# Optimization experiments

Hardware: AMD Instinct MI355X
Metric: run time of the kernel (lower is better)

## Reference

```python
import jax, jax.numpy as jnp
import numpy as np

HIDDEN_DIM = 1024
NUM_HEADS = 16
HEAD_DIM = HIDDEN_DIM // NUM_HEADS
SCALAR_NORM = float(np.sqrt(HIDDEN_DIM / NUM_HEADS))


def setup_inputs() -> dict:
    key = jax.random.key(0)
    k1, k2 = jax.random.split(key)
    B, N, D = 2, 2048, HIDDEN_DIM
    x = jax.random.normal(k1, (B, N, D), dtype=jnp.float32)
    # torch Linear weight shape: (3D, D); xavier_uniform-like scale
    limit = float(np.sqrt(6.0 / (D + 3 * D)))
    W_qkv = jax.random.uniform(k2, (3 * D, D), dtype=jnp.float32, minval=-limit, maxval=limit)
    return {"x": x, "W_qkv": W_qkv}


def reference(x, W_qkv):
    b, n, d = x.shape
    h, hd = NUM_HEADS, HEAD_DIM
    qkv = x @ W_qkv.T  # (B, N, 3D)
    q, k, v = jnp.split(qkv, 3, axis=-1)
    # (B, H, N, hd)
    q = q.reshape(b, n, h, hd).transpose(0, 2, 1, 3)
    k = k.reshape(b, n, h, hd).transpose(0, 2, 1, 3)
    v = v.reshape(b, n, h, hd).transpose(0, 2, 1, 3)
    scores = jnp.einsum('bhik,bhjk->bhij', q, k) / SCALAR_NORM
    attn = jax.nn.softmax(scores, axis=-1)
    out = jnp.einsum('bhij,bhjk->bhik', attn, v)
    return out.transpose(0, 2, 1, 3).reshape(b, n, d)
```

## Files before the change

kernel.cpp:

```cpp
#include <hip/hip_runtime.h>
#include <hip/hip_bf16.h>

#define SEQ 2048
#define DMODEL 1024
#define NHEADS 16
#define HD 64
#define BATCH 2

typedef short bf16x8 __attribute__((ext_vector_type(8)));
typedef float f32x4 __attribute__((ext_vector_type(4)));
typedef float f32x16 __attribute__((ext_vector_type(16)));

static __device__ inline ushort f2bf(float f) {
    unsigned u = __float_as_uint(f);
    return (ushort)((u + 0x7fffu + ((u >> 16) & 1u)) >> 16);
}

static __device__ inline unsigned pk2bf(float a, float b) {
    __hip_bfloat162 h = __float22bfloat162_rn(make_float2(a, b));
    union { __hip_bfloat162 h; unsigned u; } c; c.h = h;
    return c.u;
}

static __device__ inline void async16(const ushort* g, ushort* l) {
    __builtin_amdgcn_global_load_lds((const __attribute__((address_space(1))) void*)g,
                                     (__attribute__((address_space(3))) void*)l, 16, 0, 0);
}

static __device__ inline void plane32swap(unsigned& a, unsigned& b) {
    asm volatile("v_permlane32_swap_b32 %0, %1" : "+v"(a), "+v"(b));
}

__global__ void cvt2(const float* __restrict__ a, ushort* __restrict__ da, int na,
                     const float* __restrict__ b, ushort* __restrict__ db, int nb) {
    long i = (long)(blockIdx.x * blockDim.x + threadIdx.x) * 4;
    const float* s; ushort* d;
    if (i < na) { s = a + i; d = da + i; }
    else { long j = i - na; if (j >= nb) return; s = b + j; d = db + j; }
    float4 v = *(const float4*)s;
    ushort4 o; o.x = f2bf(v.x); o.y = f2bf(v.y); o.z = f2bf(v.z); o.w = f2bf(v.w);
    *(ushort4*)d = o;
}

union GemmSmem {
    struct { ushort A[128 * 64]; ushort B[128 * 64]; } st;
    ushort C[128 * 128];
};

__global__ __launch_bounds__(256) void qkv_gemm(
        const ushort* __restrict__ X, const ushort* __restrict__ W,
        ushort* __restrict__ Qd, ushort* __restrict__ Kd, ushort* __restrict__ Vd) {
    __shared__ GemmSmem sm;
    const int t = threadIdx.x;
    const int lane = t & 63, l15 = lane & 15, quad = lane >> 4;
    const int w = t >> 6, wm = w >> 1, wn = w & 1;
    const int gm = blockIdx.x, gn = blockIdx.y;
    const int srow = t >> 3, scol = (t & 7) * 8;

    f32x4 acc[4][4] = {};

    for (int kt = 0; kt < 16; ++kt) {
        const int k0 = kt * 64;
        __syncthreads();
#pragma unroll
        for (int inst = 0; inst < 4; ++inst) {
            async16(&X[(gm * 128 + inst * 32 + srow) * 1024 + k0 + scol], &sm.st.A[inst * 2048 + t * 8]);
            async16(&W[(gn * 128 + inst * 32 + srow) * 1024 + k0 + scol], &sm.st.B[inst * 2048 + t * 8]);
        }
        __syncthreads();
#pragma unroll
        for (int ks = 0; ks < 2; ++ks) {
            const int kk = ks * 32 + quad * 8;
            bf16x8 af[4], bfr[4];
#pragma unroll
            for (int i = 0; i < 4; ++i) {
                af[i]  = *(const bf16x8*)&sm.st.A[(wm * 64 + i * 16 + l15) * 64 + kk];
                bfr[i] = *(const bf16x8*)&sm.st.B[(wn * 64 + i * 16 + l15) * 64 + kk];
            }
#pragma unroll
            for (int i = 0; i < 4; ++i)
#pragma unroll
                for (int j = 0; j < 4; ++j)
                    acc[i][j] = __builtin_amdgcn_mfma_f32_16x16x32_bf16(af[i], bfr[j], acc[i][j], 0, 0, 0);
        }
    }

    __syncthreads();
    const float sc = (gn < 8) ? (0.125f * 1.44269504f) : 1.0f;
#pragma unroll
    for (int i = 0; i < 4; ++i)
#pragma unroll
        for (int reg = 0; reg < 4; ++reg) {
            const int row = wm * 64 + i * 16 + quad * 4 + reg;
            const int sw = (row & 7) * 8;
#pragma unroll
            for (int jp = 0; jp < 4; jp += 2) {
                unsigned u = pk2bf(acc[i][jp][reg] * sc, acc[i][jp + 1][reg] * sc);
                sm.C[row * 128 + ((wn * 64 + jp * 16 + l15) ^ sw)] = (ushort)u;
                sm.C[row * 128 + ((wn * 64 + (jp + 1) * 16 + l15) ^ sw)] = (ushort)(u >> 16);
            }
        }
    __syncthreads();

    const int which = gn >> 3;
    ushort* dst = (which == 0) ? Qd : ((which == 1) ? Kd : Vd);
    const int rloc = t >> 4, l = t & 15;
#pragma unroll
    for (int pass = 0; pass < 8; ++pass) {
        const int r = pass * 16 + rloc;
        bf16x8 v = *(const bf16x8*)&sm.C[r * 128 + ((l * 8) ^ ((r & 7) * 8))];
        const int ng = gm * 128 + r;
        const int b = ng >> 11, n = ng & 2047;
        const int cl = (gn * 128 + l * 8) & 1023;
        const int h = cl >> 6, hd = cl & 63;
        *(bf16x8*)&dst[(((b * NHEADS + h) * SEQ) + n) * HD + hd] = v;
    }
}

__global__ __launch_bounds__(256) void tr_v(const ushort* __restrict__ src, ushort* __restrict__ dst) {
    __shared__ ushort sT[64][72];
    const int t = threadIdx.x;
    const int bh = blockIdx.y, nt = blockIdx.x;
    const int r0 = t >> 3, c8 = (t & 7) * 8;
    const ushort* sp = src + ((long)bh * SEQ + nt * 64) * HD;
#pragma unroll
    for (int rr = 0; rr < 64; rr += 32)
        *(bf16x8*)&sT[rr + r0][c8] = *(const bf16x8*)&sp[(rr + r0) * HD + c8];
    __syncthreads();
    ushort* dp = dst + (long)bh * HD * SEQ + nt * 64;
#pragma unroll
    for (int rr = 0; rr < 64; rr += 32) {
        const int hd = rr + r0;
        bf16x8 v;
#pragma unroll
        for (int j = 0; j < 8; ++j) v[j] = (short)sT[c8 + j][hd];
        *(bf16x8*)&dp[(long)hd * SEQ + c8] = v;
    }
}

__global__ __launch_bounds__(256, 2) void attn_kernel(
        const ushort* __restrict__ Q, const ushort* __restrict__ K,
        const ushort* __restrict__ VT, float* __restrict__ O) {
    __shared__ ushort sK[2][128 * 64];
    __shared__ ushort sVT[2][64 * 128];
    __shared__ float sL[4][32];

    const int t = threadIdx.x;
    const int lane = t & 63, l31 = lane & 31, hi = lane >> 5;
    const int w = t >> 6;

    const int flat = blockIdx.y * gridDim.x + blockIdx.x;
    const int qt = (flat >> 3) & 15;
    const int bh = (flat & 7) + ((flat >> 7) << 3);

    const ushort* Qp = Q + ((long)bh * SEQ + qt * 128 + w * 32) * HD;
    const ushort* Kp = K + (long)bh * SEQ * HD;
    const ushort* Vp = VT + (long)bh * HD * SEQ;

    bf16x8 bq[4];
#pragma unroll
    for (int ks = 0; ks < 4; ++ks)
        bq[ks] = *(const bf16x8*)&Qp[l31 * HD + ks * 16 + hi * 8];

    const int krow = t >> 3;
    const int kcol = ((t & 7) ^ (krow & 7)) * 8;
    const ushort* gK = Kp + krow * HD + kcol;
    const int vrow = t >> 4;
    const int vcol = ((t & 15) ^ (vrow & 7)) * 8;
    const ushort* gV = Vp + (long)vrow * SEQ + vcol;

    ushort* lK[2] = { &sK[0][t * 8], &sK[1][t * 8] };
    ushort* lV[2] = { &sVT[0][t * 8], &sVT[1][t * 8] };

    f32x16 accO[2] = {};
    f32x4 Lp4 = {};
    const int swz = (l31 & 7) << 3;

#pragma unroll
    for (int c = 0; c < 4; ++c) {
        async16(gK + c * 32 * HD, lK[0] + c * 2048);
        async16(gV + (long)c * 16 * SEQ, lV[0] + c * 2048);
    }
    __syncthreads();

    for (int kt = 0; kt < 16; ++kt) {
        const int cur = kt & 1;
        if (kt < 15) {
            const ushort* nK = gK + (kt + 1) * 128 * HD;
            const ushort* nV = gV + (kt + 1) * 128;
#pragma unroll
            for (int c = 0; c < 4; ++c) {
                async16(nK + c * 32 * HD, lK[cur ^ 1] + c * 2048);
                async16(nV + (long)c * 16 * SEQ, lV[cur ^ 1] + c * 2048);
            }
        }
        const ushort* bK = sK[cur];
        const ushort* bV = sVT[cur];

        f32x16 s[4];
        __builtin_amdgcn_s_setprio(1);
#pragma unroll
        for (int nb = 0; nb < 4; ++nb) {
            f32x16 z = {};
#pragma unroll
            for (int ks = 0; ks < 4; ++ks) {
                bf16x8 ak = *(const bf16x8*)&bK[(nb * 32 + l31) * 64 + ((ks * 16 + hi * 8) ^ swz)];
                z = __builtin_amdgcn_mfma_f32_32x32x16_bf16(ak, bq[ks], z, 0, 0, 0);
            }
            s[nb] = z;
        }
        __builtin_amdgcn_s_setprio(0);

#pragma unroll
        for (int h = 0; h < 2; ++h) {
            bf16x8 pa[4];
#pragma unroll
            for (int nb = 0; nb < 2; ++nb) {
                float p[16];
#pragma unroll
                for (int r = 0; r < 16; ++r) p[r] = exp2f(s[h * 2 + nb][r]);
#pragma unroll
                for (int r = 0; r < 16; ++r) Lp4[r & 3] += p[r];
#pragma unroll
                for (int h2 = 0; h2 < 2; ++h2) {
                    const int b = 8 * h2;
                    unsigned c0 = pk2bf(p[b + 0], p[b + 1]);
                    unsigned c1 = pk2bf(p[b + 2], p[b + 3]);
                    unsigned c2 = pk2bf(p[b + 4], p[b + 5]);
                    unsigned c3 = pk2bf(p[b + 6], p[b + 7]);
                    plane32swap(c0, c2);
                    plane32swap(c1, c3);
                    union { unsigned u[4]; bf16x8 v; } f;
                    f.u[0] = c0; f.u[1] = c1; f.u[2] = c2; f.u[3] = c3;
                    pa[nb * 2 + h2] = f.v;
                }
            }
            __builtin_amdgcn_s_setprio(1);
#pragma unroll
            for (int db = 0; db < 2; ++db)
#pragma unroll
                for (int ks = 0; ks < 4; ++ks) {
                    bf16x8 vf = *(const bf16x8*)&bV[(db * 32 + l31) * 128 + h * 64 + ((ks * 16 + hi * 8) ^ swz)];
                    accO[db] = __builtin_amdgcn_mfma_f32_32x32x16_bf16(pa[ks], vf, accO[db], 0, 0, 0);
                }
            __builtin_amdgcn_s_setprio(0);
        }

        __syncthreads();
    }

    const float Lp = (Lp4[0] + Lp4[1]) + (Lp4[2] + Lp4[3]);
    unsigned lu = __float_as_uint(Lp), lv = lu;
    plane32swap(lu, lv);
    const float Ltot = __uint_as_float(lu) + __uint_as_float(lv);
    if (hi == 0) sL[w][l31] = Ltot;
    __syncthreads();

    const int b = bh >> 4, h = bh & 15;
    const int qg0 = qt * 128 + w * 32;
#pragma unroll
    for (int r = 0; r < 16; ++r) {
        const int ql = (r & 3) + 8 * (r >> 2) + 4 * hi;
        const float inv = 1.0f / sL[w][ql];
        const int row = qg0 + ql;
#pragma unroll
        for (int db = 0; db < 2; ++db)
            O[((long)b * SEQ + row) * DMODEL + h * HD + db * 32 + l31] = accO[db][r] * inv;
    }
}

extern "C" void kernel_launch(void* const* d_in, const int* in_sizes, int n_in,
                              void* d_out, int out_size, void* d_ws, size_t ws_size,
                              hipStream_t stream) {
    const float* x  = (const float*)d_in[0];
    const float* Wq = (const float*)d_in[1];
    float* out = (float*)d_out;

    const int NX = BATCH * SEQ * DMODEL;
    const int NW = 3 * DMODEL * DMODEL;
    const int NQKV = BATCH * NHEADS * SEQ * HD;

    ushort* xb = (ushort*)d_ws;
    ushort* wb = xb + NX;
    ushort* q  = wb + NW;
    ushort* k  = q + NQKV;
    ushort* vtmp = k + NQKV;
    ushort* vt = xb;

    cvt2<<<(NX + NW) / 4 / 256, 256, 0, stream>>>(x, xb, NX, Wq, wb, NW);

    dim3 g1(4096 / 128, 3072 / 128);
    qkv_gemm<<<g1, 256, 0, stream>>>(xb, wb, q, k, vtmp);

    dim3 gt(SEQ / 64, BATCH * NHEADS);
    tr_v<<<gt, 256, 0, stream>>>(vtmp, vt);

    dim3 g2(SEQ / 128, BATCH * NHEADS);
    attn_kernel<<<g2, 256, 0, stream>>>(q, k, vt, out);
}
```

Measured before the change: 177.7 us.

## Process two 32-row query blocks per wave to reuse K/V tile loads

```diff
diff --git a/kernel.cpp b/kernel.cpp
--- a/kernel.cpp
+++ b/kernel.cpp
@@ -138,29 +138,31 @@
     }
 }
 
-__global__ __launch_bounds__(256, 2) void attn_kernel(
+__global__ __launch_bounds__(256, 1) void attn_kernel(
         const ushort* __restrict__ Q, const ushort* __restrict__ K,
         const ushort* __restrict__ VT, float* __restrict__ O) {
     __shared__ ushort sK[2][128 * 64];
     __shared__ ushort sVT[2][64 * 128];
-    __shared__ float sL[4][32];
+    __shared__ float sL[4][64];
 
     const int t = threadIdx.x;
     const int lane = t & 63, l31 = lane & 31, hi = lane >> 5;
     const int w = t >> 6;
 
     const int flat = blockIdx.y * gridDim.x + blockIdx.x;
-    const int qt = (flat >> 3) & 15;
-    const int bh = (flat & 7) + ((flat >> 7) << 3);
-
-    const ushort* Qp = Q + ((long)bh * SEQ + qt * 128 + w * 32) * HD;
+    const int qt = (flat >> 3) & 7;
+    const int bh = (flat & 7) + ((flat >> 6) << 3);
+
+    const ushort* Qp = Q + ((long)bh * SEQ + qt * 256 + w * 64) * HD;
     const ushort* Kp = K + (long)bh * SEQ * HD;
     const ushort* Vp = VT + (long)bh * HD * SEQ;
 
-    bf16x8 bq[4];
-#pragma unroll
-    for (int ks = 0; ks < 4; ++ks)
-        bq[ks] = *(const bf16x8*)&Qp[l31 * HD + ks * 16 + hi * 8];
+    bf16x8 bq[2][4];
+#pragma unroll
+    for (int qh = 0; qh < 2; ++qh)
+#pragma unroll
+        for (int ks = 0; ks < 4; ++ks)
+            bq[qh][ks] = *(const bf16x8*)&Qp[(qh * 32 + l31) * HD + ks * 16 + hi * 8];
 
     const int krow = t >> 3;
     const int kcol = ((t & 7) ^ (krow & 7)) * 8;
@@ -172,8 +174,8 @@
     ushort* lK[2] = { &sK[0][t * 8], &sK[1][t * 8] };
     ushort* lV[2] = { &sVT[0][t * 8], &sVT[1][t * 8] };
 
-    f32x16 accO[2] = {};
-    f32x4 Lp4 = {};
+    f32x16 accA[2] = {}, accB[2] = {};
+    f32x4 LpA = {}, LpB = {};
     const int swz = (l31 & 7) << 3;
 
 #pragma unroll
@@ -197,75 +199,94 @@
         const ushort* bK = sK[cur];
         const ushort* bV = sVT[cur];
 
-        f32x16 s[4];
-        __builtin_amdgcn_s_setprio(1);
+        f32x16 sA[4], sB[4];
 #pragma unroll
         for (int nb = 0; nb < 4; ++nb) {
-            f32x16 z = {};
+            f32x16 zA = {}, zB = {};
 #pragma unroll
             for (int ks = 0; ks < 4; ++ks) {
                 bf16x8 ak = *(const bf16x8*)&bK[(nb * 32 + l31) * 64 + ((ks * 16 + hi * 8) ^ swz)];
-                z = __builtin_amdgcn_mfma_f32_32x32x16_bf16(ak, bq[ks], z, 0, 0, 0);
-            }
-            s[nb] = z;
-        }
-        __builtin_amdgcn_s_setprio(0);
+                zA = __builtin_amdgcn_mfma_f32_32x32x16_bf16(ak, bq[0][ks], zA, 0, 0, 0);
+                zB = __builtin_amdgcn_mfma_f32_32x32x16_bf16(ak, bq[1][ks], zB, 0, 0, 0);
+            }
+            sA[nb] = zA; sB[nb] = zB;
+        }
 
 #pragma unroll
         for (int h = 0; h < 2; ++h) {
-            bf16x8 pa[4];
-#pragma unroll
-            for (int nb = 0; nb < 2; ++nb) {
-                float p[16];
-#pragma unroll
-                for (int r = 0; r < 16; ++r) p[r] = exp2f(s[h * 2 + nb][r]);
-#pragma unroll
-                for (int r = 0; r < 16; ++r) Lp4[r & 3] += p[r];
+            bf16x8 paA[4], paB[4];
+#pragma unroll
+            for (int nb2 = 0; nb2 < 2; ++nb2) {
+                float pA[16], pB[16];
+#pragma unroll
+                for (int r = 0; r < 16; ++r) {
+                    pA[r] = __builtin_amdgcn_exp2f(sA[h * 2 + nb2][r]);
+                    pB[r] = __builtin_amdgcn_exp2f(sB[h * 2 + nb2][r]);
+                }
+#pragma unroll
+                for (int r = 0; r < 16; ++r) { LpA[r & 3] += pA[r]; LpB[r & 3] += pB[r]; }
 #pragma unroll
                 for (int h2 = 0; h2 < 2; ++h2) {
                     const int b = 8 * h2;
-                    unsigned c0 = pk2bf(p[b + 0], p[b + 1]);
-                    unsigned c1 = pk2bf(p[b + 2], p[b + 3]);
-                    unsigned c2 = pk2bf(p[b + 4], p[b + 5]);
-                    unsigned c3 = pk2bf(p[b + 6], p[b + 7]);
-                    plane32swap(c0, c2);
-                    plane32swap(c1, c3);
-                    union { unsigned u[4]; bf16x8 v; } f;
-                    f.u[0] = c0; f.u[1] = c1; f.u[2] = c2; f.u[3] = c3;
-                    pa[nb * 2 + h2] = f.v;
+                    unsigned a0 = pk2bf(pA[b + 0], pA[b + 1]);
+                    unsigned a1 = pk2bf(pA[b + 2], pA[b + 3]);
+                    unsigned a2 = pk2bf(pA[b + 4], pA[b + 5]);
+                    unsigned a3 = pk2bf(pA[b + 6], pA[b + 7]);
+                    plane32swap(a0, a2);
+                    plane32swap(a1, a3);
+                    union { unsigned u[4]; bf16x8 v; } fa;
+                    fa.u[0] = a0; fa.u[1] = a1; fa.u[2] = a2; fa.u[3] = a3;
+                    paA[nb2 * 2 + h2] = fa.v;
+                    unsigned b0 = pk2bf(pB[b + 0], pB[b + 1]);
+                    unsigned b1 = pk2bf(pB[b + 2], pB[b + 3]);
+                    unsigned b2 = pk2bf(pB[b + 4], pB[b + 5]);
+                    unsigned b3 = pk2bf(pB[b + 6], pB[b + 7]);
+                    plane32swap(b0, b2);
+                    plane32swap(b1, b3);
+                    union { unsigned u[4]; bf16x8 v; } fb;
+                    fb.u[0] = b0; fb.u[1] = b1; fb.u[2] = b2; fb.u[3] = b3;
+                    paB[nb2 * 2 + h2] = fb.v;
                 }
             }
-            __builtin_amdgcn_s_setprio(1);
 #pragma unroll
             for (int db = 0; db < 2; ++db)
 #pragma unroll
                 for (int ks = 0; ks < 4; ++ks) {
                     bf16x8 vf = *(const bf16x8*)&bV[(db * 32 + l31) * 128 + h * 64 + ((ks * 16 + hi * 8) ^ swz)];
-                    accO[db] = __builtin_amdgcn_mfma_f32_32x32x16_bf16(pa[ks], vf, accO[db], 0, 0, 0);
+                    accA[db] = __builtin_amdgcn_mfma_f32_32x32x16_bf16(paA[ks], vf, accA[db], 0, 0, 0);
+                    accB[db] = __builtin_amdgcn_mfma_f32_32x32x16_bf16(paB[ks], vf, accB[db], 0, 0, 0);
                 }
-            __builtin_amdgcn_s_setprio(0);
         }
 
         __syncthreads();
     }
 
-    const float Lp = (Lp4[0] + Lp4[1]) + (Lp4[2] + Lp4[3]);
-    unsigned lu = __float_as_uint(Lp), lv = lu;
-    plane32swap(lu, lv);
-    const float Ltot = __uint_as_float(lu) + __uint_as_float(lv);
-    if (hi == 0) sL[w][l31] = Ltot;
+    {
+        const float la = (LpA[0] + LpA[1]) + (LpA[2] + LpA[3]);
+        unsigned lu = __float_as_uint(la), lv = lu;
+        plane32swap(lu, lv);
+        const float lb = (LpB[0] + LpB[1]) + (LpB[2] + LpB[3]);
+        unsigned mu = __float_as_uint(lb), mv = mu;
+        plane32swap(mu, mv);
+        if (hi == 0) {
+            sL[w][l31]      = __uint_as_float(lu) + __uint_as_float(lv);
+            sL[w][32 + l31] = __uint_as_float(mu) + __uint_as_float(mv);
+        }
+    }
     __syncthreads();
 
     const int b = bh >> 4, h = bh & 15;
-    const int qg0 = qt * 128 + w * 32;
+    const int qg0 = qt * 256 + w * 64;
 #pragma unroll
     for (int r = 0; r < 16; ++r) {
         const int ql = (r & 3) + 8 * (r >> 2) + 4 * hi;
-        const float inv = 1.0f / sL[w][ql];
-        const int row = qg0 + ql;
-#pragma unroll
-        for (int db = 0; db < 2; ++db)
-            O[((long)b * SEQ + row) * DMODEL + h * HD + db * 32 + l31] = accO[db][r] * inv;
+        const float invA = 1.0f / sL[w][ql];
+        const float invB = 1.0f / sL[w][32 + ql];
+#pragma unroll
+        for (int db = 0; db < 2; ++db) {
+            O[((long)b * SEQ + qg0 + ql) * DMODEL + h * HD + db * 32 + l31]      = accA[db][r] * invA;
+            O[((long)b * SEQ + qg0 + 32 + ql) * DMODEL + h * HD + db * 32 + l31] = accB[db][r] * invB;
+        }
     }
 }
 
@@ -295,6 +316,6 @@
     dim3 gt(SEQ / 64, BATCH * NHEADS);
     tr_v<<<gt, 256, 0, stream>>>(vtmp, vt);
 
-    dim3 g2(SEQ / 128, BATCH * NHEADS);
+    dim3 g2(SEQ / 256, BATCH * NHEADS);
     attn_kernel<<<g2, 256, 0, stream>>>(q, k, vt, out);
 }
```

Result: faster. 170.1 us (-4.3%).
